# Performance work log

Hardware: AMD Instinct MI355X
Metric: run time of the kernel (lower is better)

## Reference

```python
import jax, jax.numpy as jnp
import numpy as np

N, E, D, H = 50000, 800000, 128, 8
HD = D // H  # head dim = 16


def setup_inputs() -> dict:
    key = jax.random.key(0)
    ks = jax.random.split(key, 9)
    x = jax.random.normal(ks[0], (N, D), dtype=jnp.float32)
    edge_index = jax.random.randint(ks[1], (2, E), 0, N, dtype=jnp.int64)
    s = 0.05
    Wq = jax.random.normal(ks[2], (D, D), dtype=jnp.float32) * s
    bq = jax.random.normal(ks[3], (D,), dtype=jnp.float32) * s
    Wk = jax.random.normal(ks[4], (D, D), dtype=jnp.float32) * s
    bk = jax.random.normal(ks[5], (D,), dtype=jnp.float32) * s
    Wv = jax.random.normal(ks[6], (D, D), dtype=jnp.float32) * s
    bv = jax.random.normal(ks[7], (D,), dtype=jnp.float32) * s
    return {"x": x, "Wq": Wq, "bq": bq, "Wk": Wk, "bk": bk, "Wv": Wv, "bv": bv,
            "edge_index": edge_index}


def reference(x, Wq, bq, Wk, bk, Wv, bv, edge_index):
    n = x.shape[0]
    # Linear projections (torch Linear: x @ W.T + b), split into heads
    Q = (x @ Wq.T + bq).reshape(n, H, HD)  # [N,H,hd]
    K = (x @ Wk.T + bk).reshape(n, H, HD)
    V = (x @ Wv.T + bv).reshape(n, H, HD)
    src, dst = edge_index[0], edge_index[1]
    # per-edge attention score: sum over head dim of K[src]*Q[dst]/sqrt(hd), clamp, exp
    score = jnp.sum(K[src] * Q[dst], axis=-1, keepdims=True) / np.sqrt(HD)  # [E,H,1]
    score = jnp.exp(jnp.clip(score, -5.0, 5.0))
    msg = V[src] * score  # [E,H,hd]
    wV = jax.ops.segment_sum(msg, dst, num_segments=n)      # [N,H,hd]
    Z = jax.ops.segment_sum(score, dst, num_segments=n)     # [N,H,1]
    h_out = wV / (Z + 1e-6)
    return h_out.reshape(n, H * HD)
```

## Files before the change

kernel.cpp:

```cpp
#include <hip/hip_runtime.h>
#include <hip/hip_bf16.h>

#define NN 50000
#define EE 800000
#define DD 128
#define HH 8
#define CAP 64
#define KVS 256
#define QKB 391
#define PAB 196
#define NBIN 196
#define RSTRIDE 4096

typedef short bf16x8 __attribute__((ext_vector_type(8)));
typedef float f32x4 __attribute__((ext_vector_type(4)));
typedef unsigned short ushort8_t __attribute__((ext_vector_type(8)));

__device__ __forceinline__ unsigned short f2b(float f) {
    unsigned int u = __builtin_bit_cast(unsigned int, f);
    unsigned int r = (u + 0x7FFFu + ((u >> 16) & 1u)) >> 16;
    return (unsigned short)r;
}
__device__ __forceinline__ float b2f(unsigned short u) {
    return __builtin_bit_cast(float, ((unsigned int)u) << 16);
}

__global__ __launch_bounds__(256) void prepA(const float* __restrict__ Wq,
                                             const float* __restrict__ Wk,
                                             const float* __restrict__ Wv,
                                             unsigned short* __restrict__ Wqb,
                                             unsigned short* __restrict__ Wkb,
                                             unsigned short* __restrict__ Wvb,
                                             const int* __restrict__ ei,
                                             int* __restrict__ runbuf,
                                             int* __restrict__ gcount,
                                             int* __restrict__ gstart) {
    __shared__ int lcnt[256];
    __shared__ int lpre[256];
    if (blockIdx.x < 48) {
        int idx = blockIdx.x * 256 + threadIdx.x;
        int mat = idx >> 12;
        int off = idx & 4095;
        const float* src = (mat == 0) ? Wq : (mat == 1) ? Wk : Wv;
        unsigned short* dst = (mat == 0) ? Wqb : (mat == 1) ? Wkb : Wvb;
        float4 v = ((const float4*)src)[off];
        ushort4 o;
        o.x = f2b(v.x); o.y = f2b(v.y); o.z = f2b(v.z); o.w = f2b(v.w);
        ((ushort4*)dst)[off] = o;
    } else {
        const int b = blockIdx.x - 48;
        const int t = threadIdx.x;
        lcnt[t] = 0;
        __syncthreads();

        int ss[16], dd[16], slot[16];
        int base4 = b * 1024 + t;
#pragma unroll
        for (int j = 0; j < 4; ++j) {
            int idx = base4 + j * 256;
            int4 sv = make_int4(0, 0, 0, 0);
            int4 dv = make_int4(-1, -1, -1, -1);
            if (idx < EE / 4) {
                sv = ((const int4*)ei)[idx];
                dv = ((const int4*)(ei + EE))[idx];
            }
            ss[j * 4 + 0] = sv.x; ss[j * 4 + 1] = sv.y;
            ss[j * 4 + 2] = sv.z; ss[j * 4 + 3] = sv.w;
            dd[j * 4 + 0] = dv.x; dd[j * 4 + 1] = dv.y;
            dd[j * 4 + 2] = dv.z; dd[j * 4 + 3] = dv.w;
        }
#pragma unroll
        for (int k = 0; k < 16; ++k)
            slot[k] = (dd[k] >= 0) ? atomicAdd(&lcnt[dd[k] >> 8], 1) : 0;
        __syncthreads();

        int myCnt = lcnt[t];
        lpre[t] = myCnt;
        __syncthreads();
        for (int off = 1; off < 256; off <<= 1) {
            int v = (t >= off) ? lpre[t - off] : 0;
            __syncthreads();
            lpre[t] += v;
            __syncthreads();
        }
        int excl = lpre[t] - myCnt;
        __syncthreads();
        lpre[t] = excl;
        __syncthreads();

#pragma unroll
        for (int k = 0; k < 16; ++k) {
            if (dd[k] >= 0) {
                int pos = b * RSTRIDE + lpre[dd[k] >> 8] + slot[k];
                runbuf[pos] = ss[k] | ((dd[k] & 255) << 16);
            }
        }
        if (t < NBIN) {
            gcount[t * PAB + b] = myCnt;
            gstart[t * PAB + b] = excl;
        }
    }
}

__device__ __forceinline__ void qkv_mat(const unsigned short* __restrict__ W,
                                        const float* __restrict__ bias,
                                        unsigned short* __restrict__ outp,
                                        int stride, int off,
                                        const bf16x8 a[2][4],
                                        int r0, int mrow, int kb,
                                        bool act0, bool act1) {
#pragma unroll
    for (int c0 = 0; c0 < 8; ++c0) {
        const unsigned short* wr = W + (size_t)(c0 * 16 + mrow) * DD + kb * 8;
        bf16x8 w0 = *(const bf16x8*)(wr);
        bf16x8 w1 = *(const bf16x8*)(wr + 32);
        bf16x8 w2 = *(const bf16x8*)(wr + 64);
        bf16x8 w3 = *(const bf16x8*)(wr + 96);
        float4 bv4 = *(const float4*)(bias + c0 * 16 + kb * 4);
#pragma unroll
        for (int g = 0; g < 2; ++g) {
            bool act = (g == 0) ? act0 : act1;
            f32x4 acc = {bv4.x, bv4.y, bv4.z, bv4.w};
            acc = __builtin_amdgcn_mfma_f32_16x16x32_bf16(w0, a[g][0], acc, 0, 0, 0);
            acc = __builtin_amdgcn_mfma_f32_16x16x32_bf16(w1, a[g][1], acc, 0, 0, 0);
            acc = __builtin_amdgcn_mfma_f32_16x16x32_bf16(w2, a[g][2], acc, 0, 0, 0);
            acc = __builtin_amdgcn_mfma_f32_16x16x32_bf16(w3, a[g][3], acc, 0, 0, 0);
            if (act) {
                int orow = r0 + 16 * g + mrow;
                int col = c0 * 16 + kb * 4;
                ushort4 o;
                o.x = f2b(acc[0]); o.y = f2b(acc[1]);
                o.z = f2b(acc[2]); o.w = f2b(acc[3]);
                *(ushort4*)(outp + (size_t)orow * stride + off + col) = o;
            }
        }
    }
}

__global__ __launch_bounds__(256) void qkvbin(
    const float* __restrict__ x,
    const unsigned short* __restrict__ Wq, const float* __restrict__ bq,
    const unsigned short* __restrict__ Wk, const float* __restrict__ bk,
    const unsigned short* __restrict__ Wv, const float* __restrict__ bv,
    unsigned short* __restrict__ Qb, unsigned short* __restrict__ KV,
    const int* __restrict__ runbuf, const int* __restrict__ gcount,
    const int* __restrict__ gstart, int* __restrict__ cnt,
    unsigned short* __restrict__ bucket) {
    __shared__ int cnt2[256];
    __shared__ int lpre[256];
    __shared__ int sstart[256];
    if (blockIdx.x < NBIN) {
        const int c = blockIdx.x, t = threadIdx.x;
        cnt2[t] = 0;
        int myCnt = (t < PAB) ? gcount[c * PAB + t] : 0;
        sstart[t] = (t < PAB) ? gstart[c * PAB + t] : 0;
        lpre[t] = myCnt;
        __syncthreads();
        for (int off = 1; off < 256; off <<= 1) {
            int v = (t >= off) ? lpre[t - off] : 0;
            __syncthreads();
            lpre[t] += v;
            __syncthreads();
        }
        int T = lpre[PAB - 1];
        for (int j = t; j < T; j += 256) {
            int lo = 0, hi = PAB - 1;
            while (lo < hi) {
                int mid = (lo + hi) >> 1;
                if (lpre[mid] > j) hi = mid; else lo = mid + 1;
            }
            int base = (lo > 0) ? lpre[lo - 1] : 0;
            int e = runbuf[lo * RSTRIDE + sstart[lo] + (j - base)];
            int dloc = (e >> 16) & 255;
            int p = atomicAdd(&cnt2[dloc], 1);
            if (p < CAP)
                bucket[(size_t)(c * 256 + dloc) * CAP + p] =
                    (unsigned short)(e & 0xFFFF);
        }
        __syncthreads();
        int node = c * 256 + t;
        if (node < NN) cnt[node] = cnt2[t];
    } else {
        const int b = blockIdx.x - NBIN;
        const int wave = threadIdx.x >> 6;
        const int l = threadIdx.x & 63;
        const int r0 = b * 128 + wave * 32;
        const int mrow = l & 15;
        const int kb = l >> 4;
        const bool act0 = (r0 < NN);
        const bool act1 = (r0 + 16 < NN);
        if (!act0) return;

        bf16x8 a[2][4];
#pragma unroll
        for (int g = 0; g < 2; ++g) {
            int row = (g == 0 || act1) ? (r0 + 16 * g + mrow) : r0;
            const float* xr = x + (size_t)row * DD + kb * 8;
#pragma unroll
            for (int s = 0; s < 4; ++s) {
                float4 f0 = *(const float4*)(xr + s * 32);
                float4 f1 = *(const float4*)(xr + s * 32 + 4);
                bf16x8 t;
                t[0] = (short)f2b(f0.x); t[1] = (short)f2b(f0.y);
                t[2] = (short)f2b(f0.z); t[3] = (short)f2b(f0.w);
                t[4] = (short)f2b(f1.x); t[5] = (short)f2b(f1.y);
                t[6] = (short)f2b(f1.z); t[7] = (short)f2b(f1.w);
                a[g][s] = t;
            }
        }
        qkv_mat(Wq, bq, Qb, DD, 0,    a, r0, mrow, kb, act0, act1);
        qkv_mat(Wk, bk, KV, KVS, 0,   a, r0, mrow, kb, act0, act1);
        qkv_mat(Wv, bv, KV, KVS, 128, a, r0, mrow, kb, act0, act1);
    }
}

__global__ __launch_bounds__(128) void gather8(const unsigned short* __restrict__ KV,
                                               const unsigned short* __restrict__ Qb,
                                               const int* __restrict__ cnt,
                                               const unsigned short* __restrict__ bucket,
                                               float* __restrict__ outp) {
    int n = blockIdx.x * 2 + (threadIdx.x >> 6);
    if (n >= NN) return;
    int l = threadIdx.x & 63;
    int es = l >> 3;
    int h = l & 7;

    int mySrc = (int)bucket[(size_t)n * CAP + l];
    int d = cnt[n];
    const unsigned short* qp = Qb + (size_t)n * DD + 16 * h;
    ushort8_t qu0 = *(const ushort8_t*)qp;
    ushort8_t qu1 = *(const ushort8_t*)(qp + 8);
    float qf[16];
#pragma unroll
    for (int j = 0; j < 8; ++j) qf[j] = b2f(qu0[j]);
#pragma unroll
    for (int j = 0; j < 8; ++j) qf[8 + j] = b2f(qu1[j]);

    float acc[16];
#pragma unroll
    for (int j = 0; j < 16; ++j) acc[j] = 0.f;
    float z = 0.f;
    d = min(d, CAP);

    for (int i = 0; i < d; i += 8) {
        int eidx = i + es;
        bool valid = eidx < d;
        int src = __shfl(mySrc, valid ? eidx : i);
        const unsigned short* kr = KV + (size_t)src * KVS + 16 * h;
        ushort8_t k0 = *(const ushort8_t*)kr;
        ushort8_t k1 = *(const ushort8_t*)(kr + 8);
        ushort8_t v0 = *(const ushort8_t*)(kr + 128);
        ushort8_t v1 = *(const ushort8_t*)(kr + 136);
        float s = qf[0] * b2f(k0[0]) + qf[1] * b2f(k0[1]) +
                  qf[2] * b2f(k0[2]) + qf[3] * b2f(k0[3]) +
                  qf[4] * b2f(k0[4]) + qf[5] * b2f(k0[5]) +
                  qf[6] * b2f(k0[6]) + qf[7] * b2f(k0[7]) +
                  qf[8] * b2f(k1[0]) + qf[9] * b2f(k1[1]) +
                  qf[10] * b2f(k1[2]) + qf[11] * b2f(k1[3]) +
                  qf[12] * b2f(k1[4]) + qf[13] * b2f(k1[5]) +
                  qf[14] * b2f(k1[6]) + qf[15] * b2f(k1[7]);
        s *= 0.25f;
        s = fminf(fmaxf(s, -5.f), 5.f);
        s = __expf(s);
        if (!valid) s = 0.f;
#pragma unroll
        for (int j = 0; j < 8; ++j) acc[j] += b2f(v0[j]) * s;
#pragma unroll
        for (int j = 0; j < 8; ++j) acc[8 + j] += b2f(v1[j]) * s;
        z += s;
    }
#pragma unroll
    for (int m = 8; m <= 32; m <<= 1) {
#pragma unroll
        for (int j = 0; j < 16; ++j) acc[j] += __shfl_xor(acc[j], m);
        z += __shfl_xor(z, m);
    }
    if (es == 0) {
        float inv = 1.f / (z + 1e-6f);
        float4* orow = (float4*)(outp + (size_t)n * DD + 16 * h);
#pragma unroll
        for (int j = 0; j < 4; ++j)
            orow[j] = make_float4(acc[4 * j] * inv, acc[4 * j + 1] * inv,
                                  acc[4 * j + 2] * inv, acc[4 * j + 3] * inv);
    }
}

extern "C" void kernel_launch(void* const* d_in, const int* in_sizes, int n_in,
                              void* d_out, int out_size, void* d_ws, size_t ws_size,
                              hipStream_t stream) {
    const float* x  = (const float*)d_in[0];
    const float* Wq = (const float*)d_in[1];
    const float* bq = (const float*)d_in[2];
    const float* Wk = (const float*)d_in[3];
    const float* bk = (const float*)d_in[4];
    const float* Wv = (const float*)d_in[5];
    const float* bv = (const float*)d_in[6];
    const int*   ei = (const int*)d_in[7];
    float* out = (float*)d_out;

    unsigned short* KV  = (unsigned short*)d_ws;
    unsigned short* Qb  = KV + (size_t)NN * KVS;
    unsigned short* Wqb = Qb + (size_t)NN * DD;
    unsigned short* Wkb = Wqb + DD * DD;
    unsigned short* Wvb = Wkb + DD * DD;
    int* cnt = (int*)(Wvb + DD * DD);
    unsigned short* bucket = (unsigned short*)(cnt + NN);
    int* runbuf = (int*)(bucket + (size_t)NN * CAP);
    int* gcount = runbuf + (size_t)PAB * RSTRIDE;
    int* gstart = gcount + NBIN * PAB;

    prepA<<<48 + PAB, 256, 0, stream>>>(Wq, Wk, Wv, Wqb, Wkb, Wvb, ei,
                                        runbuf, gcount, gstart);
    qkvbin<<<NBIN + QKB, 256, 0, stream>>>(x, Wqb, bq, Wkb, bk, Wvb, bv,
                                           Qb, KV, runbuf, gcount, gstart,
                                           cnt, bucket);
    gather8<<<(NN + 1) / 2, 128, 0, stream>>>(KV, Qb, cnt, bucket, out);
}
```

Before: 105.6 us.

## Store Q/K/V head-major and gather one head per block

Measured after the change: 124.1 us. 17.5% more time.

```diff
diff --git a/kernel.cpp b/kernel.cpp
--- a/kernel.cpp
+++ b/kernel.cpp
@@ -6,7 +6,6 @@
 #define DD 128
 #define HH 8
 #define CAP 64
-#define KVS 256
 #define QKB 391
 #define PAB 196
 #define NBIN 196
@@ -102,10 +101,10 @@
     }
 }
 
+template <int MODE>
 __device__ __forceinline__ void qkv_mat(const unsigned short* __restrict__ W,
                                         const float* __restrict__ bias,
                                         unsigned short* __restrict__ outp,
-                                        int stride, int off,
                                         const bf16x8 a[2][4],
                                         int r0, int mrow, int kb,
                                         bool act0, bool act1) {
@@ -127,11 +126,17 @@
             acc = __builtin_amdgcn_mfma_f32_16x16x32_bf16(w3, a[g][3], acc, 0, 0, 0);
             if (act) {
                 int orow = r0 + 16 * g + mrow;
-                int col = c0 * 16 + kb * 4;
                 ushort4 o;
                 o.x = f2b(acc[0]); o.y = f2b(acc[1]);
                 o.z = f2b(acc[2]); o.w = f2b(acc[3]);
-                *(ushort4*)(outp + (size_t)orow * stride + off + col) = o;
+                size_t addr;
+                if (MODE == 0)
+                    addr = ((size_t)c0 * NN + orow) * 16 + kb * 4;
+                else if (MODE == 1)
+                    addr = ((size_t)c0 * NN + orow) * 32 + kb * 4;
+                else
+                    addr = ((size_t)c0 * NN + orow) * 32 + 16 + kb * 4;
+                *(ushort4*)(outp + addr) = o;
             }
         }
     }
@@ -142,7 +147,7 @@
     const unsigned short* __restrict__ Wq, const float* __restrict__ bq,
     const unsigned short* __restrict__ Wk, const float* __restrict__ bk,
     const unsigned short* __restrict__ Wv, const float* __restrict__ bv,
-    unsigned short* __restrict__ Qb, unsigned short* __restrict__ KV,
+    unsigned short* __restrict__ Qh, unsigned short* __restrict__ KVh,
     const int* __restrict__ runbuf, const int* __restrict__ gcount,
     const int* __restrict__ gstart, int* __restrict__ cnt,
     unsigned short* __restrict__ bucket) {
@@ -208,26 +213,28 @@
                 a[g][s] = t;
             }
         }
-        qkv_mat(Wq, bq, Qb, DD, 0,    a, r0, mrow, kb, act0, act1);
-        qkv_mat(Wk, bk, KV, KVS, 0,   a, r0, mrow, kb, act0, act1);
-        qkv_mat(Wv, bv, KV, KVS, 128, a, r0, mrow, kb, act0, act1);
-    }
-}
-
-__global__ __launch_bounds__(128) void gather8(const unsigned short* __restrict__ KV,
-                                               const unsigned short* __restrict__ Qb,
+        qkv_mat<0>(Wq, bq, Qh,  a, r0, mrow, kb, act0, act1);
+        qkv_mat<1>(Wk, bk, KVh, a, r0, mrow, kb, act0, act1);
+        qkv_mat<2>(Wv, bv, KVh, a, r0, mrow, kb, act0, act1);
+    }
+}
+
+__global__ __launch_bounds__(256) void gatherH(const unsigned short* __restrict__ KVh,
+                                               const unsigned short* __restrict__ Qh,
                                                const int* __restrict__ cnt,
                                                const unsigned short* __restrict__ bucket,
                                                float* __restrict__ outp) {
-    int n = blockIdx.x * 2 + (threadIdx.x >> 6);
-    if (n >= NN) return;
-    int l = threadIdx.x & 63;
-    int es = l >> 3;
-    int h = l & 7;
-
-    int mySrc = (int)bucket[(size_t)n * CAP + l];
+    const int h = blockIdx.x & 7;
+    const int grp = blockIdx.x >> 3;
+    const int wave = threadIdx.x >> 6;
+    const int l = threadIdx.x & 63;
+    const int ns = l >> 4;
+    const int es = l & 15;
+    const int n = grp * 16 + wave * 4 + ns;
+
+    int mySrc = (int)bucket[(size_t)n * CAP + es];
     int d = cnt[n];
-    const unsigned short* qp = Qb + (size_t)n * DD + 16 * h;
+    const unsigned short* qp = Qh + ((size_t)h * NN + n) * 16;
     ushort8_t qu0 = *(const ushort8_t*)qp;
     ushort8_t qu1 = *(const ushort8_t*)(qp + 8);
     float qf[16];
@@ -236,21 +243,23 @@
 #pragma unroll
     for (int j = 0; j < 8; ++j) qf[8 + j] = b2f(qu1[j]);
 
+    const unsigned short* KVs = KVh + (size_t)h * NN * 32;
     float acc[16];
 #pragma unroll
     for (int j = 0; j < 16; ++j) acc[j] = 0.f;
     float z = 0.f;
     d = min(d, CAP);
 
-    for (int i = 0; i < d; i += 8) {
-        int eidx = i + es;
-        bool valid = eidx < d;
-        int src = __shfl(mySrc, valid ? eidx : i);
-        const unsigned short* kr = KV + (size_t)src * KVS + 16 * h;
-        ushort8_t k0 = *(const ushort8_t*)kr;
-        ushort8_t k1 = *(const ushort8_t*)(kr + 8);
-        ushort8_t v0 = *(const ushort8_t*)(kr + 128);
-        ushort8_t v1 = *(const ushort8_t*)(kr + 136);
+    for (int i = 0; i < d; i += 16) {
+        int slot = i + es;
+        bool valid = slot < d;
+        int src = (i == 0) ? mySrc
+                           : (int)bucket[(size_t)n * CAP + (valid ? slot : i)];
+        const unsigned short* r = KVs + (size_t)src * 32;
+        ushort8_t k0 = *(const ushort8_t*)r;
+        ushort8_t k1 = *(const ushort8_t*)(r + 8);
+        ushort8_t v0 = *(const ushort8_t*)(r + 16);
+        ushort8_t v1 = *(const ushort8_t*)(r + 24);
         float s = qf[0] * b2f(k0[0]) + qf[1] * b2f(k0[1]) +
                   qf[2] * b2f(k0[2]) + qf[3] * b2f(k0[3]) +
                   qf[4] * b2f(k0[4]) + qf[5] * b2f(k0[5]) +
@@ -270,14 +279,14 @@
         z += s;
     }
 #pragma unroll
-    for (int m = 8; m <= 32; m <<= 1) {
+    for (int m = 1; m <= 8; m <<= 1) {
 #pragma unroll
         for (int j = 0; j < 16; ++j) acc[j] += __shfl_xor(acc[j], m);
         z += __shfl_xor(z, m);
     }
     if (es == 0) {
         float inv = 1.f / (z + 1e-6f);
-        float4* orow = (float4*)(outp + (size_t)n * DD + 16 * h);
+        float4* orow = (float4*)(outp + (size_t)n * DD + h * 16);
 #pragma unroll
         for (int j = 0; j < 4; ++j)
             orow[j] = make_float4(acc[4 * j] * inv, acc[4 * j + 1] * inv,
@@ -298,9 +307,9 @@
     const int*   ei = (const int*)d_in[7];
     float* out = (float*)d_out;
 
-    unsigned short* KV  = (unsigned short*)d_ws;
-    unsigned short* Qb  = KV + (size_t)NN * KVS;
-    unsigned short* Wqb = Qb + (size_t)NN * DD;
+    unsigned short* KVh = (unsigned short*)d_ws;
+    unsigned short* Qh  = KVh + (size_t)HH * NN * 32;
+    unsigned short* Wqb = Qh + (size_t)HH * NN * 16;
     unsigned short* Wkb = Wqb + DD * DD;
     unsigned short* Wvb = Wkb + DD * DD;
     int* cnt = (int*)(Wvb + DD * DD);
@@ -312,7 +321,7 @@
     prepA<<<48 + PAB, 256, 0, stream>>>(Wq, Wk, Wv, Wqb, Wkb, Wvb, ei,
                                         runbuf, gcount, gstart);
     qkvbin<<<NBIN + QKB, 256, 0, stream>>>(x, Wqb, bq, Wkb, bk, Wvb, bv,
-                                           Qb, KV, runbuf, gcount, gstart,
+                                           Qh, KVh, runbuf, gcount, gstart,
                                            cnt, bucket);
-    gather8<<<(NN + 1) / 2, 128, 0, stream>>>(KV, Qb, cnt, bucket, out);
-}
+    gatherH<<<(NN / 16) * HH, 256, 0, stream>>>(KVh, Qh, cnt, bucket, out);
+}
```
